# Optimization experiments

Measured on AMD Instinct MI355X. Metric: run time of the kernel, lower is better.

The kernel has to match this reference:

```python
import jax, jax.numpy as jnp
import numpy as np

# Natural-order 4x4 Hadamard matrix (H @ H = 4*I); 2D inverse WHT scale = 1/16.
H4 = np.array([[1, 1, 1, 1],
               [1, -1, 1, -1],
               [1, 1, -1, -1],
               [1, -1, -1, 1]], dtype=np.float32)

B, NH, NW, C, K = 16, 28, 28, 64, 64  # out_channels=192 -> K=64 per branch


def setup_inputs() -> dict:
    key = jax.random.key(0)
    ks = jax.random.split(key, 9)
    d = {}
    for i, n in enumerate(['transIm1', 'transIm2', 'transIm3']):
        d[n] = jax.random.normal(ks[i], (16, B, NH, NW, C), dtype=jnp.float32)
    for i, n in enumerate(['weight1', 'weight2', 'weight3']):
        d[n] = jax.random.normal(ks[3 + i], (16, C, K), dtype=jnp.float32) * 0.05
    for i, n in enumerate(['bias1', 'bias2', 'bias3']):
        d[n] = jax.random.normal(ks[6 + i], (1, 1, 1, K), dtype=jnp.float32) * 0.05
    return d


def _iwht_branch(trans, w, b):
    # Per-WHT-coefficient channel matmul: [16,B,nH,nW,C] x [16,C,K] -> [16,B,nH,nW,K]
    y = jnp.einsum('tbijc,tck->tbijk', trans, w)
    _, Bb, nH, nW, Kk = y.shape
    y = y.reshape(4, 4, Bb, nH, nW, Kk)  # coeff index t = 4*u + v
    h = jnp.asarray(H4, y.dtype)
    # Inverse 2D WHT per 4x4 block, scatter blocks back to pixel grid.
    z = jnp.einsum('pu,qv,uvbijk->bipjqk', h, h, y) * (1.0 / 16.0)
    return z.reshape(Bb, 4 * nH, 4 * nW, Kk) + b


def reference(transIm1, transIm2, transIm3, weight1, weight2, weight3,
              bias1, bias2, bias3):
    out1 = _iwht_branch(transIm1, weight1, bias1)
    out2 = _iwht_branch(transIm2, weight2, bias2)
    out3 = _iwht_branch(transIm3, weight3, bias3)
    return (out1, out2, out3)
```

## Files before the change

kernel.cpp:

```cpp
#include <hip/hip_runtime.h>
#include <hip/hip_bf16.h>


typedef __attribute__((ext_vector_type(8))) short bf16x8;
typedef __attribute__((ext_vector_type(4))) float floatx4;

#define NSITES 12544
#define NTILES 784
#define OUT_PER_BRANCH 12845056
#define WT_ELEMS (3*16*64*64)
#define ROW_F 68
#define CHUNK_F (64 * ROW_F)

__device__ __forceinline__ short f32_to_bf16_bits(float f) {
    __hip_bfloat16 h = __float2bfloat16(f);
    return *reinterpret_cast<short*>(&h);
}

__global__ void transpose_weights(const float* __restrict__ w0,
                                  const float* __restrict__ w1,
                                  const float* __restrict__ w2,
                                  __hip_bfloat16* __restrict__ wT) {
    int idx = blockIdx.x * blockDim.x + threadIdx.x;
    if (idx >= WT_ELEMS) return;
    int c  = idx & 63;
    int k  = (idx >> 6) & 63;
    int t  = (idx >> 12) & 15;
    int br = idx >> 16;
    const float* w = (br == 0) ? w0 : ((br == 1) ? w1 : w2);
    wT[idx] = __float2bfloat16(w[(t * 64 + c) * 64 + k]);
}

template <bool USE_WT>
__global__ __launch_bounds__(256, 3) void iwht_kernel(
    const float* __restrict__ x0, const float* __restrict__ x1,
    const float* __restrict__ x2,
    const float* __restrict__ w0, const float* __restrict__ w1,
    const float* __restrict__ w2,
    const __hip_bfloat16* __restrict__ wT,
    const float* __restrict__ b0, const float* __restrict__ b1,
    const float* __restrict__ b2,
    float* __restrict__ out) {
    __shared__ float xs[3][CHUNK_F];

    int bx   = blockIdx.x;
    int br   = bx / NTILES;
    int tile = bx - br * NTILES;
    int lane = threadIdx.x & 63;
    int wave = threadIdx.x >> 6;
    int l15  = lane & 15;
    int quad = lane >> 4;
    int n    = wave * 16 + l15;

    const float* x    = (br == 0) ? x0 : ((br == 1) ? x1 : x2);
    const float* w    = (br == 0) ? w0 : ((br == 1) ? w1 : w2);
    const float* bias = (br == 0) ? b0 : ((br == 1) ? b1 : b2);

    const float* xg = x + (size_t)(tile * 16) * 64 + lane;

    floatx4 acc[16];
#pragma unroll
    for (int t = 0; t < 16; t++) acc[t] = (floatx4){0.f, 0.f, 0.f, 0.f};

#define STAGE(g, buf)                                                          \
    {                                                                          \
        _Pragma("unroll") for (int r = 0; r < 16; r++) {                       \
            int row = wave * 16 + r;                      \
            int tl  = row >> 4;                                                \
            int s   = row & 15;                                                \
            const float* gp = xg + ((size_t)((g) * 4 + tl) * NSITES + s) * 64; \
            __builtin_amdgcn_global_load_lds(                                  \
                (const __attribute__((address_space(1))) void*)gp,             \
                (__attribute__((address_space(3))) void*)&xs[buf][row * ROW_F],\
                4, 0, 0);                                                      \
        }                                                                      \
    }

#define COMPUTE(g, buf)                                                        \
    {                                                                          \
        _Pragma("unroll") for (int tl = 0; tl < 4; tl++) {                     \
            int t = (g) * 4 + tl;                                              \
            const float* rowp = &xs[buf][(tl * 16 + l15) * ROW_F + quad * 8];  \
            floatx4 f0 = ((const floatx4*)rowp)[0];                            \
            floatx4 f1 = ((const floatx4*)rowp)[1];                            \
            floatx4 f2 = ((const floatx4*)(rowp + 32))[0];                     \
            floatx4 f3 = ((const floatx4*)(rowp + 32))[1];                     \
            bf16x8 a0, a1;                                                     \
            _Pragma("unroll") for (int j = 0; j < 4; j++) {                    \
                a0[j]     = f32_to_bf16_bits(f0[j]);                           \
                a0[j + 4] = f32_to_bf16_bits(f1[j]);                           \
                a1[j]     = f32_to_bf16_bits(f2[j]);                           \
                a1[j + 4] = f32_to_bf16_bits(f3[j]);                           \
            }                                                                  \
            bf16x8 bb0, bb1;                                                   \
            if (USE_WT) {                                                      \
                const bf16x8* wv = reinterpret_cast<const bf16x8*>(            \
                    wT + (((size_t)(br * 16 + t) * 64 + n) * 64) + quad * 8);  \
                bb0 = wv[0];                                                   \
                bb1 = wv[4];                                                   \
            } else {                                                           \
                _Pragma("unroll") for (int j = 0; j < 8; j++) {                \
                    int c0 = quad * 8 + j;                                     \
                    bb0[j] = f32_to_bf16_bits(w[(t * 64 + c0) * 64 + n]);      \
                    bb1[j] = f32_to_bf16_bits(w[(t * 64 + c0 + 32) * 64 + n]); \
                }                                                              \
            }                                                                  \
            acc[t] = __builtin_amdgcn_mfma_f32_16x16x32_bf16(bb0, a0, acc[t],  \
                                                             0, 0, 0);         \
            acc[t] = __builtin_amdgcn_mfma_f32_16x16x32_bf16(bb1, a1, acc[t],  \
                                                             0, 0, 0);         \
        }                                                                      \
    }

#define WAITV(N)                                                               \
    asm volatile("s_waitcnt vmcnt(" #N ")" ::: "memory");                      \
    __builtin_amdgcn_s_barrier();                                              \
    __builtin_amdgcn_sched_barrier(0);

    STAGE(0, 0);
    STAGE(1, 1);
    STAGE(2, 2);

    WAITV(32);
    COMPUTE(0, 0);
    __builtin_amdgcn_s_barrier();
    STAGE(3, 0);

    WAITV(32);
    COMPUTE(1, 1);

    WAITV(16);
    COMPUTE(2, 2);

    WAITV(0);
    COMPUTE(3, 0);

#undef STAGE
#undef COMPUTE
#undef WAITV

    int k0   = wave * 16 + quad * 4;
    int site = tile * 16 + l15;
    int b    = site / 784;
    int rem  = site - b * 784;
    int i    = rem / 28;
    int j    = rem - i * 28;
    float* op = out + (size_t)br * OUT_PER_BRANCH +
                (((size_t)(b * 112 + 4 * i)) * 112 + 4 * j) * 64 + k0;
    floatx4 bias4 = *reinterpret_cast<const floatx4*>(bias + k0);

#pragma unroll
    for (int u = 0; u < 4; u++) {
        floatx4 y0 = acc[4 * u + 0], y1 = acc[4 * u + 1];
        floatx4 y2 = acc[4 * u + 2], y3 = acc[4 * u + 3];
        floatx4 A = y0 + y2, Bv = y1 + y3, Cv = y0 - y2, Dv = y1 - y3;
        acc[4 * u + 0] = A + Bv;
        acc[4 * u + 1] = A - Bv;
        acc[4 * u + 2] = Cv + Dv;
        acc[4 * u + 3] = Cv - Dv;
    }

#pragma unroll
    for (int q = 0; q < 4; q++) {
        floatx4 z0 = acc[0 + q], z1 = acc[4 + q], z2 = acc[8 + q], z3 = acc[12 + q];
        floatx4 A = z0 + z2, Bv = z1 + z3, Cv = z0 - z2, Dv = z1 - z3;
        floatx4 o[4];
        o[0] = A + Bv;
        o[1] = A - Bv;
        o[2] = Cv + Dv;
        o[3] = Cv - Dv;
#pragma unroll
        for (int p = 0; p < 4; p++) {
            floatx4 v = o[p] * 0.0625f + bias4;
            *reinterpret_cast<floatx4*>(op + (size_t)(p * 112 + q) * 64) = v;
        }
    }
}

extern "C" void kernel_launch(void* const* d_in, const int* in_sizes, int n_in,
                              void* d_out, int out_size, void* d_ws, size_t ws_size,
                              hipStream_t stream) {
    const float* x0 = (const float*)d_in[0];
    const float* x1 = (const float*)d_in[1];
    const float* x2 = (const float*)d_in[2];
    const float* w0 = (const float*)d_in[3];
    const float* w1 = (const float*)d_in[4];
    const float* w2 = (const float*)d_in[5];
    const float* b0 = (const float*)d_in[6];
    const float* b1 = (const float*)d_in[7];
    const float* b2 = (const float*)d_in[8];
    float* out = (float*)d_out;
    __hip_bfloat16* wT = (__hip_bfloat16*)d_ws;

    bool use_wt = ws_size >= (size_t)WT_ELEMS * sizeof(__hip_bfloat16);
    if (use_wt) {
        transpose_weights<<<(WT_ELEMS + 255) / 256, 256, 0, stream>>>(w0, w1, w2, wT);
        iwht_kernel<true><<<3 * NTILES, 256, 0, stream>>>(x0, x1, x2, w0, w1, w2, wT,
                                                          b0, b1, b2, out);
    } else {
        iwht_kernel<false><<<3 * NTILES, 256, 0, stream>>>(x0, x1, x2, w0, w1, w2, wT,
                                                           b0, b1, b2, out);
    }
}
```

Measured before the change: 298.3 us.

## Use 16-byte global_load_lds with XOR swizzle instead of padded 4-byte rows

Staging of the input tile into LDS switches from 4-byte per-lane global_load_lds calls into padded rows to 16-byte per-lane loads into unpadded 64-float rows. An XOR swizzle on the column index keeps LDS reads free of bank conflicts without padding. This cuts the number of load instructions per stage from 16 to 4, and the vmcnt wait thresholds are adjusted to match. It depends on 16-byte LDS-direct loads being supported and on the swizzle matching exactly between the write side and the read side.

```diff
diff --git a/kernel.cpp b/kernel.cpp
--- a/kernel.cpp
+++ b/kernel.cpp
@@ -9,8 +9,7 @@
 #define NTILES 784
 #define OUT_PER_BRANCH 12845056
 #define WT_ELEMS (3*16*64*64)
-#define ROW_F 68
-#define CHUNK_F (64 * ROW_F)
+#define CHUNK_F (64 * 64)
 
 __device__ __forceinline__ short f32_to_bf16_bits(float f) {
     __hip_bfloat16 h = __float2bfloat16(f);
@@ -56,7 +55,8 @@
     const float* w    = (br == 0) ? w0 : ((br == 1) ? w1 : w2);
     const float* bias = (br == 0) ? b0 : ((br == 1) ? b1 : b2);
 
-    const float* xg = x + (size_t)(tile * 16) * 64 + lane;
+    int sub  = lane >> 4;
+    int lcol = lane & 15;
 
     floatx4 acc[16];
 #pragma unroll
@@ -64,27 +64,30 @@
 
 #define STAGE(g, buf)                                                          \
     {                                                                          \
-        _Pragma("unroll") for (int r = 0; r < 16; r++) {                       \
-            int row = wave * 16 + r;                      \
-            int tl  = row >> 4;                                                \
-            int s   = row & 15;                                                \
-            const float* gp = xg + ((size_t)((g) * 4 + tl) * NSITES + s) * 64; \
+        _Pragma("unroll") for (int r = 0; r < 4; r++) {                        \
+            int s   = 4 * r + sub;                  \
+            int col = lcol ^ (s & 7);               \
+            const float* gp = x +                                              \
+                ((size_t)((g) * 4 + wave) * NSITES + tile * 16 + s) * 64 +     \
+                col * 4;                                                       \
             __builtin_amdgcn_global_load_lds(                                  \
                 (const __attribute__((address_space(1))) void*)gp,             \
-                (__attribute__((address_space(3))) void*)&xs[buf][row * ROW_F],\
-                4, 0, 0);                                                      \
+                (__attribute__((address_space(3))) void*)                      \
+                    &xs[buf][(wave * 16 + 4 * r) * 64],                        \
+                16, 0, 0);                                                     \
         }                                                                      \
     }
 
 #define COMPUTE(g, buf)                                                        \
     {                                                                          \
+        int xr7 = l15 & 7;                                                     \
         _Pragma("unroll") for (int tl = 0; tl < 4; tl++) {                     \
             int t = (g) * 4 + tl;                                              \
-            const float* rowp = &xs[buf][(tl * 16 + l15) * ROW_F + quad * 8];  \
-            floatx4 f0 = ((const floatx4*)rowp)[0];                            \
-            floatx4 f1 = ((const floatx4*)rowp)[1];                            \
-            floatx4 f2 = ((const floatx4*)(rowp + 32))[0];                     \
-            floatx4 f3 = ((const floatx4*)(rowp + 32))[1];                     \
+            const float* rp = &xs[buf][(tl * 16 + l15) * 64];                  \
+            floatx4 f0 = *(const floatx4*)(rp + ((quad * 2) ^ xr7) * 4);       \
+            floatx4 f1 = *(const floatx4*)(rp + ((quad * 2 + 1) ^ xr7) * 4);   \
+            floatx4 f2 = *(const floatx4*)(rp + (((quad * 2) ^ xr7) + 8) * 4); \
+            floatx4 f3 = *(const floatx4*)(rp + (((quad * 2 + 1) ^ xr7) + 8) * 4); \
             bf16x8 a0, a1;                                                     \
             _Pragma("unroll") for (int j = 0; j < 4; j++) {                    \
                 a0[j]     = f32_to_bf16_bits(f0[j]);                           \
@@ -121,15 +124,16 @@
     STAGE(1, 1);
     STAGE(2, 2);
 
-    WAITV(32);
+    WAITV(8);
     COMPUTE(0, 0);
     __builtin_amdgcn_s_barrier();
+    __builtin_amdgcn_sched_barrier(0);
     STAGE(3, 0);
 
-    WAITV(32);
+    WAITV(8);
     COMPUTE(1, 1);
 
-    WAITV(16);
+    WAITV(4);
     COMPUTE(2, 2);
 
     WAITV(0);
```

Result: no change. 296.3 us (-0.7%).
